# Kernel tuning notes

Measured on AMD Instinct MI355X. Metric: run time of the kernel, lower is better.

The kernel has to match this reference:

```python
import jax, jax.numpy as jnp
import numpy as np

T, B, IN, H, L, A = 512, 128, 544, 512, 2, 18


def setup_inputs() -> dict:
    key = jax.random.key(0)
    ks = jax.random.split(key, 16)
    s = 0.02
    return {
        "x": jax.random.normal(ks[0], (T, B, IN), jnp.float32),
        "done": jax.random.randint(ks[1], (T, B), 0, 2, jnp.int32),
        "h0": jax.random.normal(ks[2], (L, B, H), jnp.float32),
        "c0": jax.random.normal(ks[3], (L, B, H), jnp.float32),
        "W_ih0": s * jax.random.normal(ks[4], (4 * H, IN), jnp.float32),
        "W_hh0": s * jax.random.normal(ks[5], (4 * H, H), jnp.float32),
        "b_ih0": jnp.zeros((4 * H,), jnp.float32),
        "b_hh0": jnp.zeros((4 * H,), jnp.float32),
        "W_ih1": s * jax.random.normal(ks[6], (4 * H, H), jnp.float32),
        "W_hh1": s * jax.random.normal(ks[7], (4 * H, H), jnp.float32),
        "b_ih1": jnp.zeros((4 * H,), jnp.float32),
        "b_hh1": jnp.zeros((4 * H,), jnp.float32),
        "W_actor": 0.01 * jax.random.normal(ks[8], (A, H), jnp.float32),
        "b_actor": jnp.zeros((A,), jnp.float32),
        "W_critic": jax.random.normal(ks[9], (1, H), jnp.float32),
        "b_critic": jnp.zeros((1,), jnp.float32),
    }


def _lstm_cell(x, h, c, W_ih, W_hh, b_ih, b_hh):
    # PyTorch gate order: i, f, g, o
    gates = x @ W_ih.T + b_ih + h @ W_hh.T + b_hh  # [B, 4H]
    i, f, g, o = jnp.split(gates, 4, axis=-1)
    c_new = jax.nn.sigmoid(f) * c + jax.nn.sigmoid(i) * jnp.tanh(g)
    h_new = jax.nn.sigmoid(o) * jnp.tanh(c_new)
    return h_new, c_new


def reference(x, done, h0, c0, W_ih0, W_hh0, b_ih0, b_hh0,
              W_ih1, W_hh1, b_ih1, b_hh1, W_actor, b_actor, W_critic, b_critic):
    layer_params = [(W_ih0, W_hh0, b_ih0, b_hh0), (W_ih1, W_hh1, b_ih1, b_hh1)]
    done_f = done.astype(x.dtype)  # [T, B]

    def step(carry, inp):
        h, c = carry                       # each [L, B, H]
        x_t, d_t = inp                     # [B, IN], [B]
        mask = (1.0 - d_t)[None, :, None]  # reset state at episode boundary
        h = h * mask
        c = c * mask
        layer_in = x_t
        hs, cs = [], []
        for l, (Wih, Whh, bih, bhh) in enumerate(layer_params):
            h_l, c_l = _lstm_cell(layer_in, h[l], c[l], Wih, Whh, bih, bhh)
            hs.append(h_l)
            cs.append(c_l)
            layer_in = h_l
        return (jnp.stack(hs), jnp.stack(cs)), layer_in

    (h_T, c_T), hidden = jax.lax.scan(step, (h0, c0), (x, done_f))  # hidden: [T, B, H]
    hidden = hidden.reshape(-1, hidden.shape[-1])                    # [T*B, H]
    logits = hidden @ W_actor.T + b_actor                            # [T*B, A]
    value = hidden @ W_critic.T + b_critic                           # [T*B, 1]
    out = jnp.concatenate([logits, value], axis=-1)                  # [T*B, A+1]
    return out, h_T, c_T
```

## Files before the change

### kernel.cpp

```cpp
#include <hip/hip_runtime.h>
#include <hip/hip_bf16.h>


namespace {
constexpr int T = 512, B = 128, H = 512, NA = 18;
constexpr int BH = B * H;
constexpr int OUT_COLS = NA + 1;
constexpr int OUT_HT = T * B * OUT_COLS;
constexpr int OUT_CT = OUT_HT + 2 * BH;
}

using f32x4 = __attribute__((ext_vector_type(4))) float;
using s16x8 = __attribute__((ext_vector_type(8))) short;

__device__ __forceinline__ unsigned short f2bu(float f) {
  union { __hip_bfloat16 h; unsigned short u; } cv;
  cv.h = __float2bfloat16(f);
  return cv.u;
}
__device__ __forceinline__ float sigm(float x) { return 1.0f / (1.0f + __expf(-x)); }
__device__ __forceinline__ float tanh_f(float x) { return 1.0f - 2.0f / (1.0f + __expf(2.0f * x)); }

__device__ __forceinline__ void poll32(unsigned int* p) {
  for (;;) {
    unsigned int v = __hip_atomic_fetch_add(p, 0u, __ATOMIC_RELAXED, __HIP_MEMORY_SCOPE_AGENT);
    if (v >= 32u) return;
    __builtin_amdgcn_s_sleep(4);
  }
}

__device__ __forceinline__ s16x8 ld_frag_agent(const unsigned short* p) {
  const unsigned long long* q = (const unsigned long long*)p;
  unsigned long long a0 = __hip_atomic_load(q, __ATOMIC_RELAXED, __HIP_MEMORY_SCOPE_AGENT);
  unsigned long long a1 = __hip_atomic_load(q + 1, __ATOMIC_RELAXED, __HIP_MEMORY_SCOPE_AGENT);
  union { unsigned long long u[2]; s16x8 v; } r;
  r.u[0] = a0; r.u[1] = a1;
  return r.v;
}

__device__ __forceinline__ s16x8 cvt8(const float* p) {
  const f32x4* q = (const f32x4*)p;
  f32x4 a = q[0], b = q[1];
  union { s16x8 v; unsigned short u[8]; } t;
#pragma unroll
  for (int j = 0; j < 4; j++) { t.u[j] = f2bu(a[j]); t.u[4 + j] = f2bu(b[j]); }
  return t.v;
}

template <int LAYER>
__device__ void lstm_layer(const float* __restrict__ x, const int* __restrict__ done,
                           const float* __restrict__ h0in, const float* __restrict__ c0in,
                           const float* __restrict__ Wih, const float* __restrict__ Whh,
                           const float* __restrict__ bih, const float* __restrict__ bhh,
                           float* __restrict__ out, unsigned short* __restrict__ h0h,
                           unsigned short* __restrict__ h1h, unsigned int* cnt,
                           int bg, int jg, float* red, unsigned short (*hrep)[16][20]) {
  constexpr int NKCMAX = (LAYER == 0) ? 9 : 8;
  const int tid = threadIdx.x;
  const int w = tid >> 6;
  const int lane = tid & 63;
  const int lo = lane & 15;
  const int quad = lane >> 4;
  const int bbase = bg * 32, jbase = jg * 16;
  const bool rec = (w >= 2);

  int kbeg, nkc;
  if (LAYER == 0) { kbeg = (w == 0) ? 0 : (1 + w * 8); nkc = (w == 0) ? 9 : 8; }
  else            { kbeg = w * 8; nkc = 8; }

  s16x8 Bf[4][NKCMAX];
#pragma unroll
  for (int kci = 0; kci < NKCMAX; kci++) {
    if (kci < nkc) {
      int kg = (kbeg + kci) * 32 + quad * 8;
#pragma unroll
      for (int nt = 0; nt < 4; nt++) {
        int row = nt * 512 + jbase + lo;
        const float* src;
        if (LAYER == 0) src = (kg < 544) ? (Wih + (size_t)row * 544 + kg) : (Whh + (size_t)row * 512 + (kg - 544));
        else            src = (kg < 512) ? (Wih + (size_t)row * 512 + kg) : (Whh + (size_t)row * 512 + (kg - 512));
        Bf[nt][kci] = cvt8(src);
      }
    }
  }

  float bias[4];
#pragma unroll
  for (int nt = 0; nt < 4; nt++) {
    int row = nt * 512 + jbase + lo;
    bias[nt] = bih[row] + bhh[row];
  }

  const int mt = w & 1;
  const int bE0 = bbase + mt * 16 + quad * 4;
  const int jE = jbase + lo;
  float cst[4] = {0.f, 0.f, 0.f, 0.f};

  unsigned short* myh = (LAYER == 0) ? h0h : h1h;
  if (w < 2) {
#pragma unroll
    for (int r = 0; r < 4; r++) cst[r] = c0in[LAYER * BH + (bE0 + r) * 512 + jE];
    int bI = bbase + mt * 16 + (lane >> 2);
    int jI = jbase + (lane & 3) * 4;
    const float* hp = h0in + LAYER * BH + bI * 512 + jI;
    union { unsigned long long u; unsigned short s[4]; } pk;
#pragma unroll
    for (int j = 0; j < 4; j++) pk.s[j] = f2bu(hp[j]);
    __hip_atomic_store((unsigned long long*)(myh + bI * 512 + jI), pk.u,
                       __ATOMIC_RELAXED, __HIP_MEMORY_SCOPE_AGENT);
  }
  __syncthreads();

  unsigned int* c0a = cnt + (0 * 4 + bg) * 1024;
  unsigned int* c1a = cnt + (1 * 4 + bg) * 1024;
  unsigned int* cmy = (LAYER == 0) ? c0a : c1a;
  if (tid == 0) {
    __builtin_amdgcn_s_waitcnt(0);
    __hip_atomic_fetch_add(cmy + 0, 1u, __ATOMIC_RELAXED, __HIP_MEMORY_SCOPE_AGENT);
  }

  for (int t = 0; t < T; t++) {
    if (tid == 0) {
      if (LAYER == 0) {
        poll32(c0a + t);
      } else {
        poll32(c1a + t);
        poll32(c0a + t + 1);
      }
    }
    __syncthreads();

    const unsigned short* prec[2];
    const unsigned short* pin1[2];
    const float* pxf[2];
    bool dA[2];
#pragma unroll
    for (int m2 = 0; m2 < 2; m2++) {
      int b = bbase + m2 * 16 + lo;
      dA[m2] = rec ? (done[t * B + b] != 0) : false;
      if (LAYER == 0) {
        pxf[m2] = x + (size_t)(t * B + b) * 544 + quad * 8;
        prec[m2] = h0h + (size_t)t * BH + b * 512 + quad * 8;
      } else {
        pin1[m2] = h0h + (size_t)(t + 1) * BH + b * 512 + quad * 8;
        prec[m2] = h1h + (size_t)t * BH + b * 512 + quad * 8;
      }
    }
    const int koff = rec ? (kbeg - (LAYER == 0 ? 17 : 16)) * 32 : kbeg * 32;

    f32x4 acc[2][4];
#pragma unroll
    for (int m2 = 0; m2 < 2; m2++)
#pragma unroll
      for (int nt = 0; nt < 4; nt++) acc[m2][nt] = (f32x4){0.f, 0.f, 0.f, 0.f};

#pragma unroll
    for (int kci = 0; kci < NKCMAX; kci++) {
      if (kci < nkc) {
        int ko = koff + kci * 32;
#pragma unroll
        for (int m2 = 0; m2 < 2; m2++) {
          s16x8 a;
          if (rec) {
            a = ld_frag_agent(prec[m2] + ko);
            if (dA[m2]) a = s16x8{};
          } else if (LAYER == 0) {
            a = cvt8(pxf[m2] + ko);
          } else {
            a = ld_frag_agent(pin1[m2] + ko);
          }
#pragma unroll
          for (int nt = 0; nt < 4; nt++)
            acc[m2][nt] = __builtin_amdgcn_mfma_f32_16x16x32_bf16(a, Bf[nt][kci], acc[m2][nt], 0, 0, 0);
        }
      }
    }

#pragma unroll
    for (int m2 = 0; m2 < 2; m2++)
#pragma unroll
      for (int nt = 0; nt < 4; nt++)
#pragma unroll
        for (int r = 0; r < 4; r++)
          red[(((w * 2 + m2) * 16) + nt * 4 + r) * 64 + lane] = acc[m2][nt][r];
    __syncthreads();

    if (w < 2) {
      float g[4][4];
#pragma unroll
      for (int nt = 0; nt < 4; nt++)
#pragma unroll
        for (int r = 0; r < 4; r++) {
          int f = nt * 4 + r;
          g[nt][r] = red[((0 * 2 + mt) * 16 + f) * 64 + lane] + red[((1 * 2 + mt) * 16 + f) * 64 + lane] +
                     red[((2 * 2 + mt) * 16 + f) * 64 + lane] + red[((3 * 2 + mt) * 16 + f) * 64 + lane];
        }
      float hnv[4], cnv[4];
#pragma unroll
      for (int r = 0; r < 4; r++) {
        int b = bE0 + r;
        float iv = g[0][r] + bias[0];
        float fv = g[1][r] + bias[1];
        float gv = g[2][r] + bias[2];
        float ov = g[3][r] + bias[3];
        float cp = (done[t * B + b] != 0) ? 0.0f : cst[r];
        float cn = sigm(fv) * cp + sigm(iv) * tanh_f(gv);
        float hn = sigm(ov) * tanh_f(cn);
        cst[r] = cn; hnv[r] = hn; cnv[r] = cn;
        hrep[mt][quad * 4 + r][lo] = f2bu(hn);
      }
      int b2 = lane >> 2, j0l = (lane & 3) * 4;
      unsigned long long pv = *(const unsigned long long*)&hrep[mt][b2][j0l];
      int bS = bbase + mt * 16 + b2, jS = jbase + j0l;
      __hip_atomic_store((unsigned long long*)(myh + (size_t)(t + 1) * BH + bS * 512 + jS), pv,
                         __ATOMIC_RELAXED, __HIP_MEMORY_SCOPE_AGENT);
      if (t == T - 1) {
#pragma unroll
        for (int r = 0; r < 4; r++) {
          int b = bE0 + r;
          out[OUT_HT + LAYER * BH + b * 512 + jE] = hnv[r];
          out[OUT_CT + LAYER * BH + b * 512 + jE] = cnv[r];
        }
      }
    }
    __syncthreads();
    if (tid == 0) {
      __builtin_amdgcn_s_waitcnt(0);
      __hip_atomic_fetch_add(cmy + (t + 1), 1u, __ATOMIC_RELAXED, __HIP_MEMORY_SCOPE_AGENT);
    }
  }
}

__global__ __launch_bounds__(256, 1) void lstm_persist(
    const float* x, const int* done, const float* h0in, const float* c0in,
    const float* Wih0, const float* Whh0, const float* bih0, const float* bhh0,
    const float* Wih1, const float* Whh1, const float* bih1, const float* bhh1,
    float* out, unsigned short* h0h, unsigned short* h1h, unsigned int* cnt) {
  __shared__ float red[8192];
  __shared__ unsigned short hrep[2][16][20];
  const int bid = blockIdx.x;
  const int layer = bid >> 7;
  const int bl = bid & 127;
  const int bg = bl >> 5, jg = bl & 31;
  if (layer == 0)
    lstm_layer<0>(x, done, h0in, c0in, Wih0, Whh0, bih0, bhh0, out, h0h, h1h, cnt, bg, jg, red, hrep);
  else
    lstm_layer<1>(x, done, h0in, c0in, Wih1, Whh1, bih1, bhh1, out, h0h, h1h, cnt, bg, jg, red, hrep);
}

__global__ __launch_bounds__(256) void head_kernel(const unsigned short* __restrict__ hidden,
                                                   const float* __restrict__ Wa, const float* __restrict__ ba,
                                                   const float* __restrict__ Wc, const float* __restrict__ bc,
                                                   float* __restrict__ out) {
  const int tid = threadIdx.x, w = tid >> 6, lane = tid & 63, lo = lane & 15, quad = lane >> 4;
  const int mbase = blockIdx.x * 128;
  s16x8 Bf[2][16];
#pragma unroll
  for (int nt = 0; nt < 2; nt++) {
    int row = nt * 16 + lo;
#pragma unroll
    for (int kc = 0; kc < 16; kc++) {
      int kg = kc * 32 + quad * 8;
      union { s16x8 v; unsigned short u[8]; } tu;
      if (row < 18) {
        const float* s = Wa + row * 512 + kg;
#pragma unroll
        for (int j = 0; j < 8; j++) tu.u[j] = f2bu(s[j]);
      } else if (row == 18) {
        const float* s = Wc + kg;
#pragma unroll
        for (int j = 0; j < 8; j++) tu.u[j] = f2bu(s[j]);
      } else {
        tu.v = s16x8{};
      }
      Bf[nt][kc] = tu.v;
    }
  }
  f32x4 acc[2][2];
#pragma unroll
  for (int mi = 0; mi < 2; mi++)
#pragma unroll
    for (int nt = 0; nt < 2; nt++) acc[mi][nt] = (f32x4){0.f, 0.f, 0.f, 0.f};
#pragma unroll
  for (int kc = 0; kc < 16; kc++) {
#pragma unroll
    for (int mi = 0; mi < 2; mi++) {
      int m = mbase + (w * 2 + mi) * 16 + lo;
      s16x8 a = *reinterpret_cast<const s16x8*>(hidden + (size_t)m * 512 + kc * 32 + quad * 8);
      acc[mi][0] = __builtin_amdgcn_mfma_f32_16x16x32_bf16(a, Bf[0][kc], acc[mi][0], 0, 0, 0);
      acc[mi][1] = __builtin_amdgcn_mfma_f32_16x16x32_bf16(a, Bf[1][kc], acc[mi][1], 0, 0, 0);
    }
  }
  float b0 = ba[lo];
  float b1 = (lo < 2) ? ba[16 + lo] : ((lo == 2) ? bc[0] : 0.f);
#pragma unroll
  for (int mi = 0; mi < 2; mi++)
#pragma unroll
    for (int r = 0; r < 4; r++) {
      int m = mbase + (w * 2 + mi) * 16 + quad * 4 + r;
      out[(size_t)m * 19 + lo] = acc[mi][0][r] + b0;
      if (lo < 3) out[(size_t)m * 19 + 16 + lo] = acc[mi][1][r] + b1;
    }
}

extern "C" void kernel_launch(void* const* d_in, const int* in_sizes, int n_in,
                              void* d_out, int out_size, void* d_ws, size_t ws_size,
                              hipStream_t stream) {
  const float* x = (const float*)d_in[0];
  const int* done = (const int*)d_in[1];
  const float* h0 = (const float*)d_in[2];
  const float* c0 = (const float*)d_in[3];
  const float* Wih0 = (const float*)d_in[4];
  const float* Whh0 = (const float*)d_in[5];
  const float* bih0 = (const float*)d_in[6];
  const float* bhh0 = (const float*)d_in[7];
  const float* Wih1 = (const float*)d_in[8];
  const float* Whh1 = (const float*)d_in[9];
  const float* bih1 = (const float*)d_in[10];
  const float* bhh1 = (const float*)d_in[11];
  const float* Wa = (const float*)d_in[12];
  const float* ba = (const float*)d_in[13];
  const float* Wc = (const float*)d_in[14];
  const float* bc = (const float*)d_in[15];
  float* out = (float*)d_out;

  char* ws = (char*)d_ws;
  const size_t cntBytes = 32768;
  const size_t h0Off = cntBytes;
  const size_t h1Off = h0Off + (size_t)(T + 1) * BH * 2;

  unsigned int* cnt = (unsigned int*)ws;
  unsigned short* h0h = (unsigned short*)(ws + h0Off);
  unsigned short* h1h = (unsigned short*)(ws + h1Off);

  hipMemsetAsync(cnt, 0, cntBytes, stream);
  lstm_persist<<<dim3(256), dim3(256), 0, stream>>>(
      x, done, h0, c0, Wih0, Whh0, bih0, bhh0, Wih1, Whh1, bih1, bhh1,
      out, h0h, h1h, cnt);
  head_kernel<<<dim3(512), dim3(256), 0, stream>>>(h1h + BH, Wa, ba, Wc, bc, out);
}
```

Baseline: 7.517 ms.

## Make LSTM persistent-kernel sync XCD-aware with split waits and padded counters

```diff
diff --git a/kernel.cpp b/kernel.cpp
--- a/kernel.cpp
+++ b/kernel.cpp
@@ -8,6 +8,7 @@
 constexpr int OUT_COLS = NA + 1;
 constexpr int OUT_HT = T * B * OUT_COLS;
 constexpr int OUT_CT = OUT_HT + 2 * BH;
+constexpr int CSTRIDE = 16;
 }
 
 using f32x4 = __attribute__((ext_vector_type(4))) float;
@@ -21,12 +22,8 @@
 __device__ __forceinline__ float sigm(float x) { return 1.0f / (1.0f + __expf(-x)); }
 __device__ __forceinline__ float tanh_f(float x) { return 1.0f - 2.0f / (1.0f + __expf(2.0f * x)); }
 
-__device__ __forceinline__ void poll32(unsigned int* p) {
-  for (;;) {
-    unsigned int v = __hip_atomic_fetch_add(p, 0u, __ATOMIC_RELAXED, __HIP_MEMORY_SCOPE_AGENT);
-    if (v >= 32u) return;
-    __builtin_amdgcn_s_sleep(4);
-  }
+__device__ __forceinline__ unsigned rmw_peek(unsigned* p) {
+  return __hip_atomic_fetch_add(p, 0u, __ATOMIC_RELAXED, __HIP_MEMORY_SCOPE_AGENT);
 }
 
 __device__ __forceinline__ s16x8 ld_frag_agent(const unsigned short* p) {
@@ -52,9 +49,11 @@
                            const float* __restrict__ h0in, const float* __restrict__ c0in,
                            const float* __restrict__ Wih, const float* __restrict__ Whh,
                            const float* __restrict__ bih, const float* __restrict__ bhh,
-                           float* __restrict__ out, unsigned short* __restrict__ h0h,
-                           unsigned short* __restrict__ h1h, unsigned int* cnt,
-                           int bg, int jg, float* red, unsigned short (*hrep)[16][20]) {
+                           float* __restrict__ out,
+                           unsigned short* __restrict__ oloc, unsigned short* __restrict__ oifc,
+                           const unsigned short* __restrict__ iifc,
+                           unsigned* cmy, unsigned* cin, int bg, int jg, float* red,
+                           unsigned short (*hrep)[16][20], volatile unsigned* tok, bool fast) {
   constexpr int NKCMAX = (LAYER == 0) ? 9 : 8;
   const int tid = threadIdx.x;
   const int w = tid >> 6;
@@ -96,7 +95,6 @@
   const int jE = jbase + lo;
   float cst[4] = {0.f, 0.f, 0.f, 0.f};
 
-  unsigned short* myh = (LAYER == 0) ? h0h : h1h;
   if (w < 2) {
 #pragma unroll
     for (int r = 0; r < 4; r++) cst[r] = c0in[LAYER * BH + (bE0 + r) * 512 + jE];
@@ -106,31 +104,34 @@
     union { unsigned long long u; unsigned short s[4]; } pk;
 #pragma unroll
     for (int j = 0; j < 4; j++) pk.s[j] = f2bu(hp[j]);
-    __hip_atomic_store((unsigned long long*)(myh + bI * 512 + jI), pk.u,
+    size_t off0 = (size_t)bI * 512 + jI;
+    *(unsigned long long*)(oloc + off0) = pk.u;
+    __hip_atomic_store((unsigned long long*)(oifc + off0), pk.u,
                        __ATOMIC_RELAXED, __HIP_MEMORY_SCOPE_AGENT);
   }
   __syncthreads();
-
-  unsigned int* c0a = cnt + (0 * 4 + bg) * 1024;
-  unsigned int* c1a = cnt + (1 * 4 + bg) * 1024;
-  unsigned int* cmy = (LAYER == 0) ? c0a : c1a;
   if (tid == 0) {
     __builtin_amdgcn_s_waitcnt(0);
     __hip_atomic_fetch_add(cmy + 0, 1u, __ATOMIC_RELAXED, __HIP_MEMORY_SCOPE_AGENT);
   }
 
   for (int t = 0; t < T; t++) {
-    if (tid == 0) {
-      if (LAYER == 0) {
-        poll32(c0a + t);
-      } else {
-        poll32(c1a + t);
-        poll32(c0a + t + 1);
-      }
-    }
-    __syncthreads();
-
-    const unsigned short* prec[2];
+    if (rec) {
+      if (w == 2 && lane == 0) {
+        while (rmw_peek(cmy + t * CSTRIDE) < 32u) __builtin_amdgcn_s_sleep(2);
+        tok[0] = (unsigned)(t + 1);
+      }
+      while (tok[0] < (unsigned)(t + 1)) __builtin_amdgcn_s_sleep(1);
+    } else if (LAYER == 1) {
+      if (w == 0 && lane == 0) {
+        while (rmw_peek(cin + (t + 1) * CSTRIDE) < 32u) __builtin_amdgcn_s_sleep(2);
+        tok[1] = (unsigned)(t + 1);
+      }
+      while (tok[1] < (unsigned)(t + 1)) __builtin_amdgcn_s_sleep(1);
+    }
+
+    const unsigned short* precL[2];
+    const unsigned short* precI[2];
     const unsigned short* pin1[2];
     const float* pxf[2];
     bool dA[2];
@@ -138,13 +139,11 @@
     for (int m2 = 0; m2 < 2; m2++) {
       int b = bbase + m2 * 16 + lo;
       dA[m2] = rec ? (done[t * B + b] != 0) : false;
-      if (LAYER == 0) {
-        pxf[m2] = x + (size_t)(t * B + b) * 544 + quad * 8;
-        prec[m2] = h0h + (size_t)t * BH + b * 512 + quad * 8;
-      } else {
-        pin1[m2] = h0h + (size_t)(t + 1) * BH + b * 512 + quad * 8;
-        prec[m2] = h1h + (size_t)t * BH + b * 512 + quad * 8;
-      }
+      size_t roff = (size_t)t * BH + b * 512 + quad * 8;
+      precL[m2] = oloc + roff;
+      precI[m2] = oifc + roff;
+      if (LAYER == 0) pxf[m2] = x + (size_t)(t * B + b) * 544 + quad * 8;
+      else            pin1[m2] = iifc + (size_t)(t + 1) * BH + b * 512 + quad * 8;
     }
     const int koff = rec ? (kbeg - (LAYER == 0 ? 17 : 16)) * 32 : kbeg * 32;
 
@@ -162,7 +161,8 @@
         for (int m2 = 0; m2 < 2; m2++) {
           s16x8 a;
           if (rec) {
-            a = ld_frag_agent(prec[m2] + ko);
+            a = fast ? *reinterpret_cast<const s16x8*>(precL[m2] + ko)
+                     : ld_frag_agent(precI[m2] + ko);
             if (dA[m2]) a = s16x8{};
           } else if (LAYER == 0) {
             a = cvt8(pxf[m2] + ko);
@@ -212,7 +212,9 @@
       int b2 = lane >> 2, j0l = (lane & 3) * 4;
       unsigned long long pv = *(const unsigned long long*)&hrep[mt][b2][j0l];
       int bS = bbase + mt * 16 + b2, jS = jbase + j0l;
-      __hip_atomic_store((unsigned long long*)(myh + (size_t)(t + 1) * BH + bS * 512 + jS), pv,
+      size_t soff = (size_t)(t + 1) * BH + bS * 512 + jS;
+      *(unsigned long long*)(oloc + soff) = pv;
+      __hip_atomic_store((unsigned long long*)(oifc + soff), pv,
                          __ATOMIC_RELAXED, __HIP_MEMORY_SCOPE_AGENT);
       if (t == T - 1) {
 #pragma unroll
@@ -226,7 +228,7 @@
     __syncthreads();
     if (tid == 0) {
       __builtin_amdgcn_s_waitcnt(0);
-      __hip_atomic_fetch_add(cmy + (t + 1), 1u, __ATOMIC_RELAXED, __HIP_MEMORY_SCOPE_AGENT);
+      __hip_atomic_fetch_add(cmy + (t + 1) * CSTRIDE, 1u, __ATOMIC_RELAXED, __HIP_MEMORY_SCOPE_AGENT);
     }
   }
 }
@@ -235,17 +237,50 @@
     const float* x, const int* done, const float* h0in, const float* c0in,
     const float* Wih0, const float* Whh0, const float* bih0, const float* bhh0,
     const float* Wih1, const float* Whh1, const float* bih1, const float* bhh1,
-    float* out, unsigned short* h0h, unsigned short* h1h, unsigned int* cnt) {
+    float* out, unsigned short* h0loc, unsigned short* h0ifc,
+    unsigned short* h1loc, unsigned short* h1ifc,
+    unsigned* cnt, unsigned* xcc) {
   __shared__ float red[8192];
   __shared__ unsigned short hrep[2][16][20];
+  __shared__ unsigned tok[2];
+  __shared__ int sameSh;
+  const int tid = threadIdx.x;
   const int bid = blockIdx.x;
-  const int layer = bid >> 7;
-  const int bl = bid & 127;
-  const int bg = bl >> 5, jg = bl & 31;
+  const int xg = bid & 7, jg = bid >> 3;
+  const int layer = xg >> 2, bg = xg & 3;
+  const int w = tid >> 6, lane = tid & 63;
+
+  if (tid < 2) tok[tid] = 0;
+
+  unsigned* ckall = xcc + 256;
+  if (tid == 0) {
+    unsigned myxcc = 0;
+    asm volatile("s_getreg_b32 %0, hwreg(20, 0, 32)" : "=s"(myxcc));
+    __hip_atomic_store(xcc + bid, myxcc, __ATOMIC_RELAXED, __HIP_MEMORY_SCOPE_AGENT);
+    __builtin_amdgcn_s_waitcnt(0);
+    __hip_atomic_fetch_add(ckall, 1u, __ATOMIC_RELAXED, __HIP_MEMORY_SCOPE_AGENT);
+    while (rmw_peek(ckall) < 256u) __builtin_amdgcn_s_sleep(8);
+  }
+  __syncthreads();
+  if (w == 0) {
+    unsigned ref = __hip_atomic_load(xcc + bid, __ATOMIC_RELAXED, __HIP_MEMORY_SCOPE_AGENT);
+    unsigned pid = ref;
+    if (lane < 32) pid = __hip_atomic_load(xcc + (lane * 8 + xg), __ATOMIC_RELAXED, __HIP_MEMORY_SCOPE_AGENT);
+    int ok = __all((int)(pid == ref));
+    if (lane == 0) sameSh = ok;
+  }
+  __syncthreads();
+  const bool fast = (sameSh != 0);
+
+  unsigned* c0arr = cnt + (size_t)(0 + bg) * 513 * CSTRIDE;
+  unsigned* c1arr = cnt + (size_t)(4 + bg) * 513 * CSTRIDE;
+
   if (layer == 0)
-    lstm_layer<0>(x, done, h0in, c0in, Wih0, Whh0, bih0, bhh0, out, h0h, h1h, cnt, bg, jg, red, hrep);
+    lstm_layer<0>(x, done, h0in, c0in, Wih0, Whh0, bih0, bhh0, out,
+                  h0loc, h0ifc, nullptr, c0arr, nullptr, bg, jg, red, hrep, tok, fast);
   else
-    lstm_layer<1>(x, done, h0in, c0in, Wih1, Whh1, bih1, bhh1, out, h0h, h1h, cnt, bg, jg, red, hrep);
+    lstm_layer<1>(x, done, h0in, c0in, Wih1, Whh1, bih1, bhh1, out,
+                  h1loc, h1ifc, h0ifc, c1arr, c0arr, bg, jg, red, hrep, tok, fast);
 }
 
 __global__ __launch_bounds__(256) void head_kernel(const unsigned short* __restrict__ hidden,
@@ -325,17 +360,24 @@
   float* out = (float*)d_out;
 
   char* ws = (char*)d_ws;
-  const size_t cntBytes = 32768;
-  const size_t h0Off = cntBytes;
-  const size_t h1Off = h0Off + (size_t)(T + 1) * BH * 2;
-
-  unsigned int* cnt = (unsigned int*)ws;
-  unsigned short* h0h = (unsigned short*)(ws + h0Off);
-  unsigned short* h1h = (unsigned short*)(ws + h1Off);
-
-  hipMemsetAsync(cnt, 0, cntBytes, stream);
+  const size_t cntOff = 4096;
+  const size_t cntBytes = 524288;
+  const size_t HSLOT = (size_t)(T + 1) * BH * 2;
+  const size_t h0locOff = cntOff + cntBytes;
+  const size_t h0ifcOff = h0locOff + HSLOT;
+  const size_t h1locOff = h0ifcOff + HSLOT;
+  const size_t h1ifcOff = h1locOff + HSLOT;
+
+  unsigned* xcc = (unsigned*)ws;
+  unsigned* cnt = (unsigned*)(ws + cntOff);
+  unsigned short* h0loc = (unsigned short*)(ws + h0locOff);
+  unsigned short* h0ifc = (unsigned short*)(ws + h0ifcOff);
+  unsigned short* h1loc = (unsigned short*)(ws + h1locOff);
+  unsigned short* h1ifc = (unsigned short*)(ws + h1ifcOff);
+
+  hipMemsetAsync(ws, 0, cntOff + cntBytes, stream);
   lstm_persist<<<dim3(256), dim3(256), 0, stream>>>(
       x, done, h0, c0, Wih0, Whh0, bih0, bhh0, Wih1, Whh1, bih1, bhh1,
-      out, h0h, h1h, cnt);
-  head_kernel<<<dim3(512), dim3(256), 0, stream>>>(h1h + BH, Wa, ba, Wc, bc, out);
-}
+      out, h0loc, h0ifc, h1loc, h1ifc, cnt, xcc);
+  head_kernel<<<dim3(512), dim3(256), 0, stream>>>(h1loc + BH, Wa, ba, Wc, bc, out);
+}
```

Measured after the change: 6.492 ms. 13.6% less time.
